# Kernel tuning notes

Measured on AMD Instinct MI355X. Metric: run time of the kernel, lower is better.

Reference implementation:

```python
import jax, jax.numpy as jnp
import numpy as np

N_NODES = 50000
N_EDGES = 800000
D_IN, D_HID, D_LAT = 128, 128, 64
BN_EPS = 1e-5


def setup_inputs() -> dict:
    key = jax.random.key(0)
    ks = jax.random.split(key, 8)
    x = jax.random.normal(ks[0], (N_NODES, D_IN), dtype=jnp.float32)
    edge_index = jax.random.randint(ks[1], (2, N_EDGES), 0, N_NODES, dtype=jnp.int64)
    s1 = 1.0 / np.sqrt(D_IN)
    s2 = 1.0 / np.sqrt(D_HID)
    W1 = jax.random.normal(ks[2], (D_IN, D_HID), dtype=jnp.float32) * s1
    b1 = jnp.zeros((D_HID,), jnp.float32)
    gamma = jnp.ones((D_HID,), jnp.float32)
    beta = jnp.zeros((D_HID,), jnp.float32)
    Wmu = jax.random.normal(ks[3], (D_HID, D_LAT), dtype=jnp.float32) * s2
    bmu = jnp.zeros((D_LAT,), jnp.float32)
    Wls = jax.random.normal(ks[4], (D_HID, D_LAT), dtype=jnp.float32) * s2
    bls = jnp.zeros((D_LAT,), jnp.float32)
    return {"x": x, "edge_index": edge_index, "W1": W1, "b1": b1,
            "gamma": gamma, "beta": beta, "Wmu": Wmu, "bmu": bmu,
            "Wls": Wls, "bls": bls}


def _gcn_conv(h, src, dst, norm_e, inv_deg, W, b):
    # PyG GCNConv: linear transform, then sym-normalized aggregation (A+I).
    h = h @ W                                   # [N, F]
    msgs = h[src] * norm_e[:, None]             # gather + edge scaling, [E, F]
    agg = jax.ops.segment_sum(msgs, dst, num_segments=h.shape[0])
    # self-loop contribution: norm[i]*norm[i] = 1/deg[i]
    return agg + h * inv_deg[:, None] + b


def reference(x, edge_index, W1, b1, gamma, beta, Wmu, bmu, Wls, bls):
    src, dst = edge_index[0], edge_index[1]
    n = x.shape[0]
    # degrees including self loops (GCN symmetric normalization)
    deg = jax.ops.segment_sum(jnp.ones(dst.shape, x.dtype), dst, num_segments=n) + 1.0
    inv_sqrt_deg = jax.lax.rsqrt(deg)
    norm_e = inv_sqrt_deg[src] * inv_sqrt_deg[dst]   # per-edge norm, [E]
    inv_deg = 1.0 / deg

    h = _gcn_conv(x, src, dst, norm_e, inv_deg, W1, b1)
    # BatchNorm1d with batch statistics (biased var), then ReLU; dropout off (eval)
    mean = h.mean(axis=0)
    var = h.var(axis=0)
    h = (h - mean) * jax.lax.rsqrt(var + BN_EPS) * gamma + beta
    h = jax.nn.relu(h)

    mu = _gcn_conv(h, src, dst, norm_e, inv_deg, Wmu, bmu)
    log_std = _gcn_conv(h, src, dst, norm_e, inv_deg, Wls, bls)
    return mu, log_std
```

## Files before the change

kernel.cpp:

```cpp
#include <hip/hip_runtime.h>
#include <hip/hip_bf16.h>

#define N_NODES 50000
#define N_EDGES 800000
#define F 128
#define L 64
#define BN_EPS 1e-5f
#define PAD 16
#define SCAN_BLOCKS 196
#define BN_BLOCKS 391
#define EDGE_BLOCKS 3125
#define GEMM_BLOCKS 782
#define FILLB 1266

typedef __attribute__((ext_vector_type(8))) short short8;
typedef __attribute__((ext_vector_type(8))) unsigned short ushort8;
typedef __attribute__((ext_vector_type(4))) unsigned short ushortx4;
typedef __attribute__((ext_vector_type(4))) float f32x4;

static __device__ __forceinline__ float loadF(const void* p, int i, int f32) {
    if (f32) return ((const float*)p)[i];
    return __bfloat162float(((const __hip_bfloat16*)p)[i]);
}
static __device__ __forceinline__ float bfu2f(unsigned short u) {
    unsigned int t = ((unsigned int)u) << 16;
    float f;
    __builtin_memcpy(&f, &t, 4);
    return f;
}
static __device__ __forceinline__ short f2bf_s(float f) {
    union { __hip_bfloat16 b; short s; } cv;
    cv.b = __float2bfloat16(f);
    return cv.s;
}
static __device__ __forceinline__ unsigned short f2bf_u(float f) {
    union { __hip_bfloat16 b; unsigned short u; } cv;
    cv.b = __float2bfloat16(f);
    return cv.u;
}

__global__ void k_prep(const void* __restrict__ W1, const void* __restrict__ Wmu,
                       const void* __restrict__ Wls, const unsigned short* __restrict__ xs,
                       const void* __restrict__ ei, __hip_bfloat16* __restrict__ Wt1,
                       __hip_bfloat16* __restrict__ Wt2, int* __restrict__ flags,
                       int* __restrict__ degiP, int* __restrict__ src32,
                       int* __restrict__ dst32) {
    int b = blockIdx.x;
    int t = threadIdx.x;
    if (b == 0) {
        __shared__ int cnt[2];
        if (t < 2) cnt[t] = 0;
        __syncthreads();
        unsigned short v = xs[2 * t];
        int e = (v >> 7) & 0xff;
        int sane = (e >= 112 && e <= 133) ? 1 : 0;
        if (v == 0 || v == 0x8000) sane = 1;
        atomicAdd(&cnt[0], sane);
        atomicAdd(&cnt[1], (((const int*)ei)[2 * t + 1] != 0) ? 1 : 0);
        __syncthreads();
        if (t == 0) {
            flags[0] = (cnt[0] < 128) ? 1 : 0;
            flags[1] = (cnt[1] < 8) ? 1 : 0;
            flags[2] = 0;
        }
    } else if (b <= 64) {
        __shared__ int cnt;
        if (t == 0) cnt = 0;
        __syncthreads();
        unsigned short v = ((const unsigned short*)W1)[2 * t];
        int e = (v >> 7) & 0xff;
        atomicAdd(&cnt, (e >= 100 && e <= 133) ? 1 : 0);
        __syncthreads();
        int f32 = (cnt < 128) ? 1 : 0;
        int idx = (b - 1) * 256 + t;
        int n = idx >> 7, k = idx & 127;
        Wt1[idx] = __float2bfloat16(loadF(W1, k * F + n, f32));
        float v2 = (n < L) ? loadF(Wmu, k * L + n, f32) : loadF(Wls, k * L + (n - L), f32);
        Wt2[idx] = __float2bfloat16(v2);
    } else {
        int e0 = (b - 65) * 256 + t;
        __shared__ int nz;
        if (t == 0) nz = 0;
        __syncthreads();
        int w = ((const int*)ei)[2 * e0 + 1];
        if (w != 0) atomicAdd(&nz, 1);
        __syncthreads();
        int d;
        if (nz < 8) {
            int s = (int)((const long long*)ei)[e0];
            d = (int)((const long long*)ei)[N_EDGES + e0];
            src32[e0] = s;
            dst32[e0] = d;
        } else {
            d = ((const int*)ei)[N_EDGES + e0];
        }
        atomicAdd(&degiP[d * PAD], 1);
    }
}

__global__ void k_offs_alloc(const int* __restrict__ degiP, int* __restrict__ flags,
                             int* __restrict__ offsP, float* __restrict__ isd) {
    __shared__ int s[256];
    __shared__ int base;
    int t = threadIdx.x;
    int i = blockIdx.x * 256 + t;
    int v = (i < N_NODES) ? degiP[i * PAD] : 0;
    s[t] = v;
    __syncthreads();
    for (int o = 1; o < 256; o <<= 1) {
        int u = (t >= o) ? s[t - o] : 0;
        __syncthreads();
        s[t] += u;
        __syncthreads();
    }
    if (t == 255) base = atomicAdd(&flags[2], s[255]);
    __syncthreads();
    if (i < N_NODES) {
        offsP[i * PAD] = base + s[t] - v;
        isd[i] = 1.0f / sqrtf((float)v + 1.0f);
    }
}

static __device__ __forceinline__ void gemm_body(int bid, const void* __restrict__ Xin,
        const __hip_bfloat16* __restrict__ Wt, const float* __restrict__ isd,
        const int* __restrict__ flags, int mode,
        const float* __restrict__ bnscale, const float* __restrict__ bnshift,
        unsigned short* __restrict__ outb) {
    int wave = threadIdx.x >> 6, lane = threadIdx.x & 63;
    int quad = lane >> 4, mr = lane & 15;
    int m0 = bid * 64 + wave * 16;
    int node = m0 + mr;
    int row = (node < N_NODES) ? node : N_NODES - 1;
    short8 a[4];
    if (mode == 1) {
        const unsigned short* xb = (const unsigned short*)Xin;
#pragma unroll
        for (int t = 0; t < 4; ++t) {
            int k0 = t * 32 + quad * 8;
            ushort8 raw = *(const ushort8*)(xb + row * F + k0);
            f32x4 s0 = *(const f32x4*)(bnscale + k0);
            f32x4 s1 = *(const f32x4*)(bnscale + k0 + 4);
            f32x4 h0 = *(const f32x4*)(bnshift + k0);
            f32x4 h1 = *(const f32x4*)(bnshift + k0 + 4);
            short8 av;
#pragma unroll
            for (int j = 0; j < 4; ++j)
                av[j] = f2bf_s(fmaxf(bfu2f(raw[j]) * s0[j] + h0[j], 0.f));
#pragma unroll
            for (int j = 0; j < 4; ++j)
                av[4 + j] = f2bf_s(fmaxf(bfu2f(raw[4 + j]) * s1[j] + h1[j], 0.f));
            a[t] = av;
        }
    } else if (flags[0]) {
        const float* xf = (const float*)Xin;
#pragma unroll
        for (int t = 0; t < 4; ++t) {
            int off = row * F + t * 32 + quad * 8;
            f32x4 v0 = *(const f32x4*)(xf + off);
            f32x4 v1 = *(const f32x4*)(xf + off + 4);
            short8 av;
#pragma unroll
            for (int j = 0; j < 4; ++j) av[j] = f2bf_s(v0[j]);
#pragma unroll
            for (int j = 0; j < 4; ++j) av[4 + j] = f2bf_s(v1[j]);
            a[t] = av;
        }
    } else {
        const short* xb = (const short*)Xin;
#pragma unroll
        for (int t = 0; t < 4; ++t)
            a[t] = *(const short8*)(xb + row * F + t * 32 + quad * 8);
    }
    f32x4 acc[8];
    const short* wb = (const short*)Wt;
#pragma unroll
    for (int nt = 0; nt < 8; ++nt) {
        const short* wp = wb + (nt * 16 + mr) * F + quad * 8;
        f32x4 c = {0.f, 0.f, 0.f, 0.f};
        c = __builtin_amdgcn_mfma_f32_16x16x32_bf16(*(const short8*)(wp), a[0], c, 0, 0, 0);
        c = __builtin_amdgcn_mfma_f32_16x16x32_bf16(*(const short8*)(wp + 32), a[1], c, 0, 0, 0);
        c = __builtin_amdgcn_mfma_f32_16x16x32_bf16(*(const short8*)(wp + 64), a[2], c, 0, 0, 0);
        c = __builtin_amdgcn_mfma_f32_16x16x32_bf16(*(const short8*)(wp + 96), a[3], c, 0, 0, 0);
        acc[nt] = c;
    }
    if (node < N_NODES) {
        float sd = isd[node];
        unsigned short* op = outb + node * F;
#pragma unroll
        for (int nt = 0; nt < 8; ++nt) {
            ushortx4 r;
#pragma unroll
            for (int j = 0; j < 4; ++j) r[j] = f2bf_u(acc[nt][j] * sd);
            *(ushortx4*)(op + nt * 16 + quad * 4) = r;
        }
    }
}

__global__ __launch_bounds__(256) void k_fill_gemm1(
        const int* __restrict__ ei32, const int* __restrict__ src32,
        const int* __restrict__ dst32, const int* __restrict__ flags,
        int* __restrict__ offsP, int* __restrict__ csr,
        const void* __restrict__ X, const __hip_bfloat16* __restrict__ Wt1,
        const float* __restrict__ isd, unsigned short* __restrict__ outb) {
    if (blockIdx.x < GEMM_BLOCKS) {
        gemm_body(blockIdx.x, X, Wt1, isd, flags, 0, nullptr, nullptr, outb);
    } else {
        const int* sp;
        const int* dp;
        if (flags[1]) { sp = src32; dp = dst32; }
        else          { sp = ei32;  dp = ei32 + N_EDGES; }
        int stride = FILLB * 256;
        for (int e = (blockIdx.x - GEMM_BLOCKS) * 256 + threadIdx.x; e < N_EDGES;
             e += stride) {
            int d = dp[e];
            int pos = atomicAdd(&offsP[d * PAD], 1);
            csr[pos] = sp[e];
        }
    }
}

__global__ __launch_bounds__(256) void k_gemm_bn(const void* __restrict__ Xin,
        const __hip_bfloat16* __restrict__ Wt, const float* __restrict__ isd,
        const int* __restrict__ flags, const float* __restrict__ bnscale,
        const float* __restrict__ bnshift, unsigned short* __restrict__ outb) {
    gemm_body(blockIdx.x, Xin, Wt, isd, flags, 1, bnscale, bnshift, outb);
}

static __device__ __forceinline__ void agg_accum(int node, int grp, int l16,
        const ushort8* __restrict__ vp, const int* __restrict__ csr,
        const int* __restrict__ offsP, const int* __restrict__ degiP, float acc[8]) {
#pragma unroll
    for (int j = 0; j < 8; ++j) acc[j] = 0.f;
    if (grp == 0) {
        ushort8 u = vp[node * 16 + l16];
#pragma unroll
        for (int j = 0; j < 8; ++j) acc[j] = bfu2f(u[j]);
    }
    int end = offsP[node * PAD];
    int start = end - degiP[node * PAD];
    int i = start + grp;
    for (; i + 12 < end; i += 16) {
        ushort8 u0 = vp[csr[i] * 16 + l16];
        ushort8 u1 = vp[csr[i + 4] * 16 + l16];
        ushort8 u2 = vp[csr[i + 8] * 16 + l16];
        ushort8 u3 = vp[csr[i + 12] * 16 + l16];
#pragma unroll
        for (int j = 0; j < 8; ++j)
            acc[j] += (bfu2f(u0[j]) + bfu2f(u1[j])) + (bfu2f(u2[j]) + bfu2f(u3[j]));
    }
    for (; i + 4 < end; i += 8) {
        ushort8 u0 = vp[csr[i] * 16 + l16];
        ushort8 u1 = vp[csr[i + 4] * 16 + l16];
#pragma unroll
        for (int j = 0; j < 8; ++j) acc[j] += bfu2f(u0[j]) + bfu2f(u1[j]);
    }
    for (; i < end; i += 4) {
        ushort8 u = vp[csr[i] * 16 + l16];
#pragma unroll
        for (int j = 0; j < 8; ++j) acc[j] += bfu2f(u[j]);
    }
#pragma unroll
    for (int j = 0; j < 8; ++j) {
        acc[j] += __shfl_xor(acc[j], 16);
        acc[j] += __shfl_xor(acc[j], 32);
    }
}

__global__ void k_agg1(const unsigned short* __restrict__ val, const int* __restrict__ csr,
                       const int* __restrict__ offsP, const int* __restrict__ degiP,
                       const float* __restrict__ isd, const void* __restrict__ b1,
                       const int* __restrict__ flags, unsigned short* __restrict__ out) {
    int node = blockIdx.x * 4 + (threadIdx.x >> 6);
    if (node >= N_NODES) return;
    int lane = threadIdx.x & 63;
    int grp = lane >> 4, l16 = lane & 15;
    float acc[8];
    agg_accum(node, grp, l16, (const ushort8*)val, csr, offsP, degiP, acc);
    if (grp == 0) {
        float sd = isd[node];
        int c0 = l16 * 8, f32 = flags[0];
        ushort8 r;
#pragma unroll
        for (int j = 0; j < 8; ++j) r[j] = f2bf_u(acc[j] * sd + loadF(b1, c0 + j, f32));
        ((ushort8*)out)[node * 16 + l16] = r;
    }
}

__global__ void k_bnstats(const unsigned short* __restrict__ h, float* __restrict__ partial) {
    __shared__ float ls[256][8];
    __shared__ float lq[256][8];
    int t = threadIdx.x;
    int o = t & 15, rg = t >> 4;
    int row0 = blockIdx.x * 128 + rg;
    float s[8] = {0.f}, q[8] = {0.f};
#pragma unroll
    for (int i = 0; i < 8; ++i) {
        int row = row0 + i * 16;
        if (row < N_NODES) {
            ushort8 u = *(const ushort8*)(h + row * F + o * 8);
#pragma unroll
            for (int j = 0; j < 8; ++j) {
                float v = bfu2f(u[j]);
                s[j] += v;
                q[j] += v * v;
            }
        }
    }
#pragma unroll
    for (int j = 0; j < 8; ++j) { ls[t][j] = s[j]; lq[t][j] = q[j]; }
    __syncthreads();
    if (t < 128) {
        int c = t, oo = c >> 3, jj = c & 7;
        float ts = 0.f, tq = 0.f;
#pragma unroll
        for (int rgi = 0; rgi < 16; ++rgi) {
            ts += ls[rgi * 16 + oo][jj];
            tq += lq[rgi * 16 + oo][jj];
        }
        partial[blockIdx.x * 256 + c] = ts;
        partial[blockIdx.x * 256 + 128 + c] = tq;
    }
}

__global__ void k_bnredprep(const float* __restrict__ partial, const void* __restrict__ gamma,
                            const void* __restrict__ beta, const int* __restrict__ flags,
                            float* __restrict__ scale, float* __restrict__ shift) {
    int c = blockIdx.x;
    float s = 0.f, q = 0.f;
    for (int b = threadIdx.x; b < BN_BLOCKS; b += 256) {
        s += partial[b * 256 + c];
        q += partial[b * 256 + 128 + c];
    }
#pragma unroll
    for (int o = 32; o; o >>= 1) {
        s += __shfl_down(s, o);
        q += __shfl_down(q, o);
    }
    __shared__ float ws[4], wq[4];
    if ((threadIdx.x & 63) == 0) {
        ws[threadIdx.x >> 6] = s;
        wq[threadIdx.x >> 6] = q;
    }
    __syncthreads();
    if (threadIdx.x == 0) {
        float S = ws[0] + ws[1] + ws[2] + ws[3];
        float Q = wq[0] + wq[1] + wq[2] + wq[3];
        const float invN = 1.0f / (float)N_NODES;
        float m = S * invN;
        float var = Q * invN - m * m;
        int f32 = flags[0];
        float sc = loadF(gamma, c, f32) * rsqrtf(var + BN_EPS);
        scale[c] = sc;
        shift[c] = loadF(beta, c, f32) - m * sc;
    }
}

__global__ void k_agg2(const unsigned short* __restrict__ val, const int* __restrict__ csr,
                       const int* __restrict__ offsP, const int* __restrict__ degiP,
                       const float* __restrict__ isd, const void* __restrict__ bmu,
                       const void* __restrict__ bls, const int* __restrict__ flags,
                       void* __restrict__ out) {
    int node = blockIdx.x * 4 + (threadIdx.x >> 6);
    if (node >= N_NODES) return;
    int lane = threadIdx.x & 63;
    int grp = lane >> 4, l16 = lane & 15;
    float acc[8];
    agg_accum(node, grp, l16, (const ushort8*)val, csr, offsP, degiP, acc);
    if (grp == 0) {
        float sd = isd[node];
        int c0 = l16 * 8, f32 = flags[0];
        int hsel = (c0 >= L) ? 1 : 0;
        int cc = c0 - hsel * L;
        const void* bp = hsel ? bls : bmu;
        float o8[8];
#pragma unroll
        for (int j = 0; j < 8; ++j) o8[j] = acc[j] * sd + loadF(bp, cc + j, f32);
        long base_o = (long)hsel * (N_NODES * 64) + (long)node * 64 + cc;
        if (f32) {
            f32x4 r0 = {o8[0], o8[1], o8[2], o8[3]};
            f32x4 r1 = {o8[4], o8[5], o8[6], o8[7]};
            __builtin_nontemporal_store(r0, (f32x4*)((float*)out + base_o));
            __builtin_nontemporal_store(r1, (f32x4*)((float*)out + base_o + 4));
        } else {
            ushort8 r;
#pragma unroll
            for (int j = 0; j < 8; ++j) r[j] = f2bf_u(o8[j]);
            __builtin_nontemporal_store(r, (ushort8*)((__hip_bfloat16*)out + base_o));
        }
    }
}

extern "C" void kernel_launch(void* const* d_in, const int* in_sizes, int n_in,
                              void* d_out, int out_size, void* d_ws, size_t ws_size,
                              hipStream_t stream) {
    const void* x     = d_in[0];
    const void* ei    = d_in[1];
    const void* W1    = d_in[2];
    const void* b1    = d_in[3];
    const void* gamma = d_in[4];
    const void* beta  = d_in[5];
    const void* Wmu   = d_in[6];
    const void* bmu   = d_in[7];
    const void* Wls   = d_in[8];
    const void* bls   = d_in[9];

    int*   degiP = (int*)d_ws;
    int*   offsP = degiP + N_NODES * PAD;
    float* isd   = (float*)(offsP + N_NODES * PAD);
    float* stats = isd + 50048;
    int*   flags = (int*)(stats + 512);
    int*   csr   = flags + 16;
    int*   src32 = csr + 800000;
    int*   dst32 = src32 + 800000;
    __hip_bfloat16* Wt1 = (__hip_bfloat16*)(dst32 + 800000);
    __hip_bfloat16* Wt2 = Wt1 + 16384;
    unsigned short* Abf = (unsigned short*)(Wt2 + 16384);
    unsigned short* Hpre = Abf + N_NODES * F;
    float* partial = (float*)(Hpre + N_NODES * F);

    const int NT = 256;
    const int AGG_BLOCKS = (N_NODES + 3) / 4;

    hipMemsetAsync(degiP, 0, (size_t)N_NODES * PAD * sizeof(int), stream);
    k_prep<<<65 + EDGE_BLOCKS, NT, 0, stream>>>(W1, Wmu, Wls, (const unsigned short*)x,
                                                ei, Wt1, Wt2, flags, degiP, src32, dst32);
    k_offs_alloc<<<SCAN_BLOCKS, NT, 0, stream>>>(degiP, flags, offsP, isd);
    k_fill_gemm1<<<GEMM_BLOCKS + FILLB, NT, 0, stream>>>(
        (const int*)ei, src32, dst32, flags, offsP, csr, x, Wt1, isd, Abf);
    k_agg1<<<AGG_BLOCKS, NT, 0, stream>>>(Abf, csr, offsP, degiP, isd, b1, flags, Hpre);
    k_bnstats<<<BN_BLOCKS, NT, 0, stream>>>(Hpre, partial);
    k_bnredprep<<<128, NT, 0, stream>>>(partial, gamma, beta, flags, stats, stats + 128);
    k_gemm_bn<<<GEMM_BLOCKS, NT, 0, stream>>>(Hpre, Wt2, isd, flags, stats, stats + 128, Abf);
    k_agg2<<<AGG_BLOCKS, NT, 0, stream>>>(Abf, csr, offsP, degiP, isd, bmu, bls, flags, d_out);
}
```

Baseline: 314.9 us.

## Build CSR from per-edge atomic ranks with partitioned atomic-free fill

The degree-count pass now records each edge's atomic return value as its rank, so the CSR fill writes csr[offs[d]+rank[e]] with no second round of atomics. The fill blocks are split into 8 destination-range partitions, each scanning all edges and writing only the destinations in its range, which aims to localise scattered writes. The padded per-node counters (PAD 16) are replaced by dense arrays, which shrinks the memset and the strided reads but puts neighbouring counters in the same cache lines during the degree atomics. The cost is an extra 3.2MB rank buffer and reading the edge list 8 times in the fill.

```diff
diff --git a/kernel.cpp b/kernel.cpp
--- a/kernel.cpp
+++ b/kernel.cpp
@@ -6,12 +6,14 @@
 #define F 128
 #define L 64
 #define BN_EPS 1e-5f
-#define PAD 16
 #define SCAN_BLOCKS 196
 #define BN_BLOCKS 391
 #define EDGE_BLOCKS 3125
 #define GEMM_BLOCKS 782
-#define FILLB 1266
+#define NPART 8
+#define PART_SZ 6250
+#define SUBS 158
+#define FILLB 1264
 
 typedef __attribute__((ext_vector_type(8))) short short8;
 typedef __attribute__((ext_vector_type(8))) unsigned short ushort8;
@@ -43,8 +45,8 @@
                        const void* __restrict__ Wls, const unsigned short* __restrict__ xs,
                        const void* __restrict__ ei, __hip_bfloat16* __restrict__ Wt1,
                        __hip_bfloat16* __restrict__ Wt2, int* __restrict__ flags,
-                       int* __restrict__ degiP, int* __restrict__ src32,
-                       int* __restrict__ dst32) {
+                       int* __restrict__ degi, int* __restrict__ src32,
+                       int* __restrict__ dst32, int* __restrict__ rank) {
     int b = blockIdx.x;
     int t = threadIdx.x;
     if (b == 0) {
@@ -94,17 +96,17 @@
         } else {
             d = ((const int*)ei)[N_EDGES + e0];
         }
-        atomicAdd(&degiP[d * PAD], 1);
-    }
-}
-
-__global__ void k_offs_alloc(const int* __restrict__ degiP, int* __restrict__ flags,
-                             int* __restrict__ offsP, float* __restrict__ isd) {
+        rank[e0] = atomicAdd(&degi[d], 1);
+    }
+}
+
+__global__ void k_offs_alloc(const int* __restrict__ degi, int* __restrict__ flags,
+                             int* __restrict__ offs, float* __restrict__ isd) {
     __shared__ int s[256];
     __shared__ int base;
     int t = threadIdx.x;
     int i = blockIdx.x * 256 + t;
-    int v = (i < N_NODES) ? degiP[i * PAD] : 0;
+    int v = (i < N_NODES) ? degi[i] : 0;
     s[t] = v;
     __syncthreads();
     for (int o = 1; o < 256; o <<= 1) {
@@ -116,7 +118,7 @@
     if (t == 255) base = atomicAdd(&flags[2], s[255]);
     __syncthreads();
     if (i < N_NODES) {
-        offsP[i * PAD] = base + s[t] - v;
+        offs[i] = base + s[t] - v;
         isd[i] = 1.0f / sqrtf((float)v + 1.0f);
     }
 }
@@ -198,8 +200,9 @@
 
 __global__ __launch_bounds__(256) void k_fill_gemm1(
         const int* __restrict__ ei32, const int* __restrict__ src32,
-        const int* __restrict__ dst32, const int* __restrict__ flags,
-        int* __restrict__ offsP, int* __restrict__ csr,
+        const int* __restrict__ dst32, const int* __restrict__ rank,
+        const int* __restrict__ flags, const int* __restrict__ offs,
+        int* __restrict__ csr,
         const void* __restrict__ X, const __hip_bfloat16* __restrict__ Wt1,
         const float* __restrict__ isd, unsigned short* __restrict__ outb) {
     if (blockIdx.x < GEMM_BLOCKS) {
@@ -209,12 +212,13 @@
         const int* dp;
         if (flags[1]) { sp = src32; dp = dst32; }
         else          { sp = ei32;  dp = ei32 + N_EDGES; }
-        int stride = FILLB * 256;
-        for (int e = (blockIdx.x - GEMM_BLOCKS) * 256 + threadIdx.x; e < N_EDGES;
-             e += stride) {
+        int grp = blockIdx.x & (NPART - 1);
+        int sub = (blockIdx.x - GEMM_BLOCKS) >> 3;
+        int lo = grp * PART_SZ, hi = lo + PART_SZ;
+        int stride = SUBS * 256;
+        for (int e = sub * 256 + threadIdx.x; e < N_EDGES; e += stride) {
             int d = dp[e];
-            int pos = atomicAdd(&offsP[d * PAD], 1);
-            csr[pos] = sp[e];
+            if (d >= lo && d < hi) csr[offs[d] + rank[e]] = sp[e];
         }
     }
 }
@@ -228,7 +232,7 @@
 
 static __device__ __forceinline__ void agg_accum(int node, int grp, int l16,
         const ushort8* __restrict__ vp, const int* __restrict__ csr,
-        const int* __restrict__ offsP, const int* __restrict__ degiP, float acc[8]) {
+        const int* __restrict__ offs, const int* __restrict__ degi, float acc[8]) {
 #pragma unroll
     for (int j = 0; j < 8; ++j) acc[j] = 0.f;
     if (grp == 0) {
@@ -236,8 +240,8 @@
 #pragma unroll
         for (int j = 0; j < 8; ++j) acc[j] = bfu2f(u[j]);
     }
-    int end = offsP[node * PAD];
-    int start = end - degiP[node * PAD];
+    int start = offs[node];
+    int end = start + degi[node];
     int i = start + grp;
     for (; i + 12 < end; i += 16) {
         ushort8 u0 = vp[csr[i] * 16 + l16];
@@ -267,7 +271,7 @@
 }
 
 __global__ void k_agg1(const unsigned short* __restrict__ val, const int* __restrict__ csr,
-                       const int* __restrict__ offsP, const int* __restrict__ degiP,
+                       const int* __restrict__ offs, const int* __restrict__ degi,
                        const float* __restrict__ isd, const void* __restrict__ b1,
                        const int* __restrict__ flags, unsigned short* __restrict__ out) {
     int node = blockIdx.x * 4 + (threadIdx.x >> 6);
@@ -275,7 +279,7 @@
     int lane = threadIdx.x & 63;
     int grp = lane >> 4, l16 = lane & 15;
     float acc[8];
-    agg_accum(node, grp, l16, (const ushort8*)val, csr, offsP, degiP, acc);
+    agg_accum(node, grp, l16, (const ushort8*)val, csr, offs, degi, acc);
     if (grp == 0) {
         float sd = isd[node];
         int c0 = l16 * 8, f32 = flags[0];
@@ -356,7 +360,7 @@
 }
 
 __global__ void k_agg2(const unsigned short* __restrict__ val, const int* __restrict__ csr,
-                       const int* __restrict__ offsP, const int* __restrict__ degiP,
+                       const int* __restrict__ offs, const int* __restrict__ degi,
                        const float* __restrict__ isd, const void* __restrict__ bmu,
                        const void* __restrict__ bls, const int* __restrict__ flags,
                        void* __restrict__ out) {
@@ -365,7 +369,7 @@
     int lane = threadIdx.x & 63;
     int grp = lane >> 4, l16 = lane & 15;
     float acc[8];
-    agg_accum(node, grp, l16, (const ushort8*)val, csr, offsP, degiP, acc);
+    agg_accum(node, grp, l16, (const ushort8*)val, csr, offs, degi, acc);
     if (grp == 0) {
         float sd = isd[node];
         int c0 = l16 * 8, f32 = flags[0];
@@ -404,15 +408,16 @@
     const void* Wls   = d_in[8];
     const void* bls   = d_in[9];
 
-    int*   degiP = (int*)d_ws;
-    int*   offsP = degiP + N_NODES * PAD;
-    float* isd   = (float*)(offsP + N_NODES * PAD);
+    int*   degi  = (int*)d_ws;
+    int*   offs  = degi + 50048;
+    float* isd   = (float*)(offs + 50048);
     float* stats = isd + 50048;
     int*   flags = (int*)(stats + 512);
     int*   csr   = flags + 16;
     int*   src32 = csr + 800000;
     int*   dst32 = src32 + 800000;
-    __hip_bfloat16* Wt1 = (__hip_bfloat16*)(dst32 + 800000);
+    int*   rank  = dst32 + 800000;
+    __hip_bfloat16* Wt1 = (__hip_bfloat16*)(rank + 800000);
     __hip_bfloat16* Wt2 = Wt1 + 16384;
     unsigned short* Abf = (unsigned short*)(Wt2 + 16384);
     unsigned short* Hpre = Abf + N_NODES * F;
@@ -421,15 +426,16 @@
     const int NT = 256;
     const int AGG_BLOCKS = (N_NODES + 3) / 4;
 
-    hipMemsetAsync(degiP, 0, (size_t)N_NODES * PAD * sizeof(int), stream);
+    hipMemsetAsync(degi, 0, 50048 * sizeof(int), stream);
     k_prep<<<65 + EDGE_BLOCKS, NT, 0, stream>>>(W1, Wmu, Wls, (const unsigned short*)x,
-                                                ei, Wt1, Wt2, flags, degiP, src32, dst32);
-    k_offs_alloc<<<SCAN_BLOCKS, NT, 0, stream>>>(degiP, flags, offsP, isd);
+                                                ei, Wt1, Wt2, flags, degi, src32, dst32,
+                                                rank);
+    k_offs_alloc<<<SCAN_BLOCKS, NT, 0, stream>>>(degi, flags, offs, isd);
     k_fill_gemm1<<<GEMM_BLOCKS + FILLB, NT, 0, stream>>>(
-        (const int*)ei, src32, dst32, flags, offsP, csr, x, Wt1, isd, Abf);
-    k_agg1<<<AGG_BLOCKS, NT, 0, stream>>>(Abf, csr, offsP, degiP, isd, b1, flags, Hpre);
+        (const int*)ei, src32, dst32, rank, flags, offs, csr, x, Wt1, isd, Abf);
+    k_agg1<<<AGG_BLOCKS, NT, 0, stream>>>(Abf, csr, offs, degi, isd, b1, flags, Hpre);
     k_bnstats<<<BN_BLOCKS, NT, 0, stream>>>(Hpre, partial);
     k_bnredprep<<<128, NT, 0, stream>>>(partial, gamma, beta, flags, stats, stats + 128);
     k_gemm_bn<<<GEMM_BLOCKS, NT, 0, stream>>>(Hpre, Wt2, isd, flags, stats, stats + 128, Abf);
-    k_agg2<<<AGG_BLOCKS, NT, 0, stream>>>(Abf, csr, offsP, degiP, isd, bmu, bls, flags, d_out);
-}
+    k_agg2<<<AGG_BLOCKS, NT, 0, stream>>>(Abf, csr, offs, degi, isd, bmu, bls, flags, d_out);
+}
```

New measurement: 286.4 us, median of 2. 9.1% less time.
